# Optimization experiments

Hardware: AMD Instinct MI355X
Metric: run time of the kernel (lower is better)

The kernel has to match this reference:

```python
import jax, jax.numpy as jnp
import numpy as np
from jax.ops import segment_sum, segment_max

N, E, F, H, G, P, C = 50000, 600000, 128, 128, 64, 32, 10
HEADS = 3
BN_EPS = 1e-5
COS_EPS = 1e-8


def setup_inputs() -> dict:
    key = jax.random.key(0)
    ks = jax.random.split(key, 32)
    rn = lambda k, shape, s: jax.random.normal(k, shape, jnp.float32) * s
    inp = {
        "x": jax.random.normal(ks[0], (N, F), jnp.float32),
        "edge_index": jax.random.randint(ks[1], (2, E), 0, N, jnp.int32),
        "batch": jnp.sort(jax.random.randint(ks[2], (N,), 0, G, jnp.int32)),
        # GCNConv
        "W1": rn(ks[3], (F, H), F ** -0.5), "b1": jnp.zeros((H,), jnp.float32),
        # SAGEConv (lin_l on aggregated neighbors, lin_r on root)
        "Wl": rn(ks[4], (H, H), H ** -0.5), "Wr": rn(ks[5], (H, H), H ** -0.5),
        "bs": jnp.zeros((H,), jnp.float32),
        # GATConv, heads=3, concat=False
        "Wg": rn(ks[6], (H, HEADS * H), H ** -0.5),
        "a_src": rn(ks[7], (HEADS, H), H ** -0.5),
        "a_dst": rn(ks[8], (HEADS, H), H ** -0.5),
        "bg": jnp.zeros((H,), jnp.float32),
        # prototype head / classifier / decoder
        "protos": jax.random.normal(ks[9], (P, H), jnp.float32),
        "Wc": rn(ks[10], (H, C), H ** -0.5), "bc": jnp.zeros((C,), jnp.float32),
        "Wd1": rn(ks[11], (H, 2 * H), H ** -0.5), "bd1": jnp.zeros((2 * H,), jnp.float32),
        "Wd2": rn(ks[12], (2 * H, F), (2 * H) ** -0.5), "bd2": jnp.zeros((F,), jnp.float32),
    }
    # BatchNorm (eval mode): gamma, beta, running mean/var for bn1..bn3
    for i in range(3):
        k0, k1, k2 = jax.random.split(ks[13 + i], 3)
        inp[f"g{i+1}"] = 1.0 + rn(k0, (H,), 0.05)
        inp[f"be{i+1}"] = rn(k1, (H,), 0.05)
        inp[f"m{i+1}"] = rn(k2, (H,), 0.1)
        inp[f"v{i+1}"] = jnp.ones((H,), jnp.float32)
    return inp


def _bn(x, g, b, m, v):
    return (x - m) * jax.lax.rsqrt(v + BN_EPS) * g + b


def _forward(x, edge_index, batch,
             W1, b1, g1, be1, m1, v1,
             Wl, Wr, bs, g2, be2, m2, v2,
             Wg, a_src, a_dst, bg, g3, be3, m3, v3,
             protos, Wc, bc, Wd1, bd1, Wd2, bd2):
    src, dst = edge_index[0], edge_index[1]
    ones_e = jnp.ones((src.shape[0],), x.dtype)

    # --- GCNConv: symmetric norm with self-loops ---
    h = x @ W1                                        # [N, H]
    deg = segment_sum(ones_e, dst, num_segments=N) + 1.0
    dinv = jax.lax.rsqrt(deg)
    coef = dinv[src] * dinv[dst]                      # [E]
    h1 = segment_sum(h[src] * coef[:, None], dst, num_segments=N)
    h1 = h1 + h * (dinv * dinv)[:, None] + b1         # self-loop term + bias
    h1 = jax.nn.elu(_bn(h1, g1, be1, m1, v1))         # dropout = identity (eval)

    # --- SAGEConv: mean aggregation (no self-loops) ---
    cnt = segment_sum(ones_e, dst, num_segments=N)
    mean_nb = segment_sum(h1[src], dst, num_segments=N) / jnp.maximum(cnt, 1.0)[:, None]
    h2 = mean_nb @ Wl + h1 @ Wr + bs
    h2 = jax.nn.elu(_bn(h2, g2, be2, m2, v2))

    # --- GATConv: heads=3, concat=False (mean), with self-loops ---
    hg = (h2 @ Wg).reshape(N, HEADS, H)               # [N, 3, H]
    al_src = jnp.einsum('nhf,hf->nh', hg, a_src)      # [N, 3]
    al_dst = jnp.einsum('nhf,hf->nh', hg, a_dst)
    loop = jnp.arange(N, dtype=src.dtype)
    s2 = jnp.concatenate([src, loop])
    d2 = jnp.concatenate([dst, loop])
    e = jax.nn.leaky_relu(al_src[s2] + al_dst[d2], 0.2)   # [E+N, 3]
    emax = segment_max(e, d2, num_segments=N)             # every node has a self-loop
    ex = jnp.exp(e - emax[d2])
    den = segment_sum(ex, d2, num_segments=N)
    alpha = ex / den[d2]                                  # [E+N, 3]
    h3 = segment_sum(hg[s2] * alpha[:, :, None], d2, num_segments=N)
    h3 = h3.mean(axis=1) + bg                             # concat=False -> head mean
    h3 = jax.nn.elu(_bn(h3, g3, be3, m3, v3))

    # --- global mean pool over graphs ---
    gcnt = segment_sum(jnp.ones((N,), x.dtype), batch, num_segments=G)
    pooled = segment_sum(h3, batch, num_segments=G) / jnp.maximum(gcnt, 1.0)[:, None]

    # --- prototype head: cosine sim -> softmax -> mix ---
    xn = pooled / jnp.maximum(jnp.linalg.norm(pooled, axis=-1, keepdims=True), COS_EPS)
    pn = protos / jnp.maximum(jnp.linalg.norm(protos, axis=-1, keepdims=True), COS_EPS)
    sims = xn @ pn.T                                      # [G, P]
    assignments = jax.nn.softmax(sims, axis=-1)
    proto_emb = assignments @ protos                      # [G, H]
    logits = proto_emb @ Wc + bc                          # [G, C]
    reconstructed = jax.nn.relu(pooled @ Wd1 + bd1) @ Wd2 + bd2   # [G, F]
    return logits, proto_emb, assignments, reconstructed


def reference(x, edge_index, batch,
              W1, b1, g1, be1, m1, v1,
              Wl, Wr, bs, g2, be2, m2, v2,
              Wg, a_src, a_dst, bg, g3, be3, m3, v3,
              protos, Wc, bc, Wd1, bd1, Wd2, bd2):
    return _forward(x, edge_index, batch,
                    W1, b1, g1, be1, m1, v1,
                    Wl, Wr, bs, g2, be2, m2, v2,
                    Wg, a_src, a_dst, bg, g3, be3, m3, v3,
                    protos, Wc, bc, Wd1, bd1, Wd2, bd2)
```

## Files before the change

kernel.cpp:

```cpp
#include <hip/hip_runtime.h>
#include <hip/hip_bf16.h>
#include <stdint.h>
#include <stddef.h>

#define N_ 50000
#define E_ 600000
#define F_ 128
#define H_ 128
#define G_ 64
#define P_ 32
#define C_ 10
#define NB_ 49

typedef __hip_bfloat16 bf16;
typedef __attribute__((ext_vector_type(8))) short short8;
typedef __attribute__((ext_vector_type(4))) float float4v;

__device__ __forceinline__ float us2f(unsigned short u){ return __uint_as_float(((unsigned int)u)<<16); }
__device__ __forceinline__ unsigned short f2us(float x){ bf16 h = __float2bfloat16(x); return *(unsigned short*)&h; }
__device__ __forceinline__ float blo(unsigned int u){ return __uint_as_float(u<<16); }
__device__ __forceinline__ float bhi(unsigned int u){ return __uint_as_float(u & 0xFFFF0000u); }
__device__ __forceinline__ unsigned int packbf(float lo, float hi){ return ((unsigned int)f2us(hi)<<16) | f2us(lo); }
__device__ __forceinline__ float eluf(float x){ return x>0.f ? x : __expf(x)-1.f; }
__device__ __forceinline__ float bnf(float x,float m,float v,float g,float b){ return (x-m)*rsqrtf(v+1e-5f)*g+b; }
__device__ __forceinline__ float lrelu(float x){ return x>0.f ? x : 0.2f*x; }
__device__ __forceinline__ float expc(float x){ return __expf(fminf(x, 50.f)); }
__device__ __forceinline__ void atomAddF(float* a, float v){ unsafeAtomicAdd(a, v); }

__global__ __launch_bounds__(256) void k_wprep(const float* __restrict__ W1, const float* __restrict__ Wl,
    const float* __restrict__ Wr, const float* __restrict__ Wg, unsigned short* __restrict__ WT){
  int idx = blockIdx.x*256 + threadIdx.x;
  if(idx >= 6*16384) return;
  int m    = idx >> 14;
  int tile = (idx >> 11) & 7;
  int kc   = (idx >> 9) & 3;
  int lane = (idx >> 3) & 63;
  int j    = idx & 7;
  int k = kc*32 + (lane>>4)*8 + j;
  int n = tile*16 + (lane&15);
  float v;
  if(m==0)      v = W1[k*128+n];
  else if(m==1) v = Wl[k*128+n];
  else if(m==2) v = Wr[k*128+n];
  else          v = Wg[k*384 + (m-3)*128 + n];
  WT[idx] = f2us(v);
}

__global__ __launch_bounds__(384) void k_vprep(const float* __restrict__ Wg, const float* __restrict__ a_src,
    const float* __restrict__ a_dst, float* __restrict__ vs3, float* __restrict__ vd3){
  int t = threadIdx.x;
  if(t >= 384) return;
  int h = t >> 7, f = t & 127;
  const float4* wr = (const float4*)(Wg + (size_t)f*384 + h*128);
  const float4* as = (const float4*)(a_src + h*128);
  const float4* ad = (const float4*)(a_dst + h*128);
  float s = 0.f, d = 0.f;
  #pragma unroll 8
  for(int j=0;j<32;j++){
    float4 wv = wr[j], av = as[j], dv = ad[j];
    s += wv.x*av.x + wv.y*av.y + wv.z*av.z + wv.w*av.w;
    d += wv.x*dv.x + wv.y*dv.y + wv.z*dv.z + wv.w*dv.w;
  }
  vs3[t] = s; vd3[t] = d;
}

__device__ __forceinline__ void load_Afrag_bf16(const bf16* A, int row, int lane, short8 af[4]){
  const unsigned short* ap = (const unsigned short*)A + (size_t)row*128 + (lane>>4)*8;
  #pragma unroll
  for(int kc=0;kc<4;kc++) af[kc] = *(const short8*)(ap + kc*32);
}
__device__ __forceinline__ void mfma_pass_g(const unsigned short* __restrict__ WB, const short8 af[4],
                                            int lane, float4v acc[8]){
  #pragma unroll
  for(int tile=0;tile<8;tile++){
    #pragma unroll
    for(int kc=0;kc<4;kc++){
      short8 bfv = *(const short8*)(WB + (((tile*4+kc)*64 + lane)<<3));
      acc[tile] = __builtin_amdgcn_mfma_f32_16x16x32_bf16(af[kc], bfv, acc[tile], 0, 0, 0);
    }
  }
}

__global__ __launch_bounds__(256) void k_mm_x(const float* __restrict__ X, const unsigned short* __restrict__ WTg,
                                              bf16* __restrict__ HB){
  const int tid = threadIdx.x, lane = tid&63, w = tid>>6;
  const int row0 = blockIdx.x*64;
  int arow = row0 + w*16 + (lane&15);
  int ar = arow < N_ ? arow : N_-1;
  const float* ap = X + (size_t)ar*128 + (lane>>4)*8;
  short8 af[4];
  #pragma unroll
  for(int kc=0;kc<4;kc++){
    float4 a = *(const float4*)(ap + kc*32);
    float4 b = *(const float4*)(ap + kc*32 + 4);
    short8 v;
    v[0]=(short)f2us(a.x); v[1]=(short)f2us(a.y); v[2]=(short)f2us(a.z); v[3]=(short)f2us(a.w);
    v[4]=(short)f2us(b.x); v[5]=(short)f2us(b.y); v[6]=(short)f2us(b.z); v[7]=(short)f2us(b.w);
    af[kc]=v;
  }
  float4v acc[8];
  #pragma unroll
  for(int t=0;t<8;t++){ acc[t][0]=0.f; acc[t][1]=0.f; acc[t][2]=0.f; acc[t][3]=0.f; }
  mfma_pass_g(WTg, af, lane, acc);
  const int colb = lane&15, q = lane>>4;
  unsigned short* ob = (unsigned short*)HB;
  #pragma unroll
  for(int r=0;r<4;r++){
    int ro = row0 + w*16 + q*4 + r;
    if(ro < N_){
      #pragma unroll
      for(int tile=0;tile<8;tile++)
        ob[(size_t)ro*128 + tile*16 + colb] = f2us(acc[tile][r]);
    }
  }
}

__global__ __launch_bounds__(256) void k_sage_mm_att(const bf16* __restrict__ MaB, const bf16* __restrict__ H1B,
    const unsigned short* __restrict__ WlF, const unsigned short* __restrict__ WrF,
    const float* __restrict__ bs, const float* __restrict__ g2, const float* __restrict__ be2,
    const float* __restrict__ m2, const float* __restrict__ v2,
    const float* __restrict__ vs3, const float* __restrict__ vd3,
    bf16* __restrict__ H2B, float* __restrict__ als3, float* __restrict__ ald3){
  const int tid = threadIdx.x, lane = tid&63, w = tid>>6;
  const int row0 = blockIdx.x*64;
  int arow = row0 + w*16 + (lane&15);
  int ar = arow < N_ ? arow : N_-1;
  float4v acc[8];
  #pragma unroll
  for(int t=0;t<8;t++){ acc[t][0]=0.f; acc[t][1]=0.f; acc[t][2]=0.f; acc[t][3]=0.f; }
  short8 af[4];
  load_Afrag_bf16(MaB, ar, lane, af);
  mfma_pass_g(WlF, af, lane, acc);
  load_Afrag_bf16(H1B, ar, lane, af);
  mfma_pass_g(WrF, af, lane, acc);

  const int colb = lane&15, q = lane>>4;
  float vsv[24], vdv[24];
  #pragma unroll
  for(int h=0;h<3;h++){
    #pragma unroll
    for(int tile=0;tile<8;tile++){
      vsv[h*8+tile] = vs3[h*128 + tile*16 + colb];
      vdv[h*8+tile] = vd3[h*128 + tile*16 + colb];
    }
  }
  unsigned short* ob = (unsigned short*)H2B;
  #pragma unroll
  for(int tile=0;tile<8;tile++){
    int col = tile*16 + colb;
    float bsv=bs[col], gv=g2[col], bev=be2[col], mv=m2[col], vv=v2[col];
    #pragma unroll
    for(int r=0;r<4;r++){
      int ro = row0 + w*16 + q*4 + r;
      float x = eluf(bnf(acc[tile][r] + bsv, mv, vv, gv, bev));
      acc[tile][r] = x;
      if(ro < N_) ob[(size_t)ro*128 + col] = f2us(x);
    }
  }
  #pragma unroll
  for(int r=0;r<4;r++){
    int ro = row0 + w*16 + q*4 + r;
    #pragma unroll
    for(int h=0;h<3;h++){
      float ps=0.f, pd=0.f;
      #pragma unroll
      for(int tile=0;tile<8;tile++){ ps += acc[tile][r]*vsv[h*8+tile]; pd += acc[tile][r]*vdv[h*8+tile]; }
      #pragma unroll
      for(int o=8;o>0;o>>=1){ ps += __shfl_down(ps,o,16); pd += __shfl_down(pd,o,16); }
      if(colb==0 && ro<N_){ als3[ro*3+h] = ps; ald3[ro*3+h] = pd; }
    }
  }
}

__global__ __launch_bounds__(256) void k_gat_mm3(const bf16* __restrict__ U, const unsigned short* __restrict__ WgF,
    const float* __restrict__ bg, const float* __restrict__ g3, const float* __restrict__ be3,
    const float* __restrict__ m3, const float* __restrict__ v3, bf16* __restrict__ H3B){
  const int tid = threadIdx.x, lane = tid&63, w = tid>>6;
  const int row0 = blockIdx.x*64;
  int arow = row0 + w*16 + (lane&15);
  int ar = arow < N_ ? arow : N_-1;
  float4v acc[8];
  #pragma unroll
  for(int t=0;t<8;t++){ acc[t][0]=0.f; acc[t][1]=0.f; acc[t][2]=0.f; acc[t][3]=0.f; }
  short8 af[4];
  for(int hh=0; hh<3; hh++){
    const unsigned short* ap = (const unsigned short*)U + (size_t)ar*384 + hh*128 + (lane>>4)*8;
    #pragma unroll
    for(int kc=0;kc<4;kc++) af[kc] = *(const short8*)(ap + kc*32);
    mfma_pass_g(WgF + hh*16384, af, lane, acc);
  }
  const int colb = lane&15, q = lane>>4;
  unsigned short* ob = (unsigned short*)H3B;
  #pragma unroll
  for(int tile=0;tile<8;tile++){
    int col = tile*16 + colb;
    float bgv=bg[col], gv=g3[col], bev=be3[col], mv=m3[col], vv=v3[col];
    #pragma unroll
    for(int r=0;r<4;r++){
      int ro = row0 + w*16 + q*4 + r;
      if(ro < N_){
        float x = acc[tile][r] + bgv;
        ob[(size_t)ro*128 + col] = f2us(eluf(bnf(x, mv, vv, gv, bev)));
      }
    }
  }
}

__global__ __launch_bounds__(256) void k_count(const int* __restrict__ dst, int* __restrict__ cnt){
  int e = blockIdx.x*256 + threadIdx.x;
  if(e < E_) atomicAdd(&cnt[dst[e]], 1);
}

__global__ __launch_bounds__(1024) void k_scan1(const int* __restrict__ cnt, int* __restrict__ row_ptr,
                                                float* __restrict__ dinv, int* __restrict__ bsum){
  __shared__ int wsum[16];
  const int t = threadIdx.x, lane = t & 63, wid = t >> 6;
  int i = blockIdx.x*1024 + t;
  int v = (i<N_) ? cnt[i] : 0;
  int x = v;
  #pragma unroll
  for(int o=1;o<64;o<<=1){
    int y = __shfl_up(x, o, 64);
    if(lane >= o) x += y;
  }
  if(lane==63) wsum[wid] = x;
  __syncthreads();
  if(wid==0){
    int s = (lane<16) ? wsum[lane] : 0;
    #pragma unroll
    for(int o=1;o<16;o<<=1){
      int y = __shfl_up(s, o, 64);
      if(lane >= o) s += y;
    }
    if(lane<16) wsum[lane] = s;
  }
  __syncthreads();
  int waveoff = (wid>0) ? wsum[wid-1] : 0;
  int incl = waveoff + x;
  if(i<N_){
    row_ptr[i] = incl - v;
    dinv[i] = rsqrtf((float)v + 1.f);
  }
  if(t==1023) bsum[blockIdx.x] = incl;
}

__global__ __launch_bounds__(64) void k_scan2(const int* __restrict__ bsum, int* __restrict__ boff,
                                              int* __restrict__ row_ptr){
  int lane = threadIdx.x;
  int v = (lane < NB_) ? bsum[lane] : 0;
  int x = v;
  #pragma unroll
  for(int o=1;o<64;o<<=1){
    int y = __shfl_up(x, o, 64);
    if(lane >= o) x += y;
  }
  if(lane < NB_) boff[lane] = x - v;
  if(lane == 63) row_ptr[N_] = x;
}

__global__ __launch_bounds__(256) void k_scan3(int* __restrict__ row_ptr, const int* __restrict__ boff,
                                               int* __restrict__ tmp){
  int i = blockIdx.x*256 + threadIdx.x;
  if(i < N_){
    int r = row_ptr[i] + boff[i>>10];
    row_ptr[i] = r;
    tmp[i] = r;
  }
}

__global__ __launch_bounds__(256) void k_scatter(const int* __restrict__ src, const int* __restrict__ dst,
                                                 int* __restrict__ tmp, int* __restrict__ esrc,
                                                 int* __restrict__ edst){
  int e = blockIdx.x*256 + threadIdx.x;
  if(e < E_){
    int d = dst[e];
    int pos = atomicAdd(&tmp[d], 1);
    esrc[pos] = src[e];
    edst[pos] = d;
  }
}

__global__ __launch_bounds__(256) void k_wexp(const int* __restrict__ esrc, const int* __restrict__ edst,
    const float* __restrict__ als3, const float* __restrict__ ald3, float* __restrict__ we4){
  int e = blockIdx.x*256 + threadIdx.x;
  if(e >= E_) return;
  int s = esrc[e], d = edst[e];
  float4 w;
  w.x = expc(lrelu(als3[s*3+0] + ald3[d*3+0]));
  w.y = expc(lrelu(als3[s*3+1] + ald3[d*3+1]));
  w.z = expc(lrelu(als3[s*3+2] + ald3[d*3+2]));
  w.w = 0.f;
  *(float4*)(we4 + (size_t)e*4) = w;
}

__global__ __launch_bounds__(256) void k_gcn_gather(const int* __restrict__ row_ptr, const int* __restrict__ esrc,
    const float* __restrict__ dinv, const bf16* __restrict__ HB,
    const float* __restrict__ b1, const float* __restrict__ g1, const float* __restrict__ be1,
    const float* __restrict__ m1, const float* __restrict__ v1, bf16* __restrict__ H1B){
  int n = blockIdx.x*4 + (threadIdx.x>>6);
  int lane = threadIdx.x & 63;
  if(n >= N_) return;
  int beg = row_ptr[n], end = row_ptr[n+1];
  float dn = dinv[n];
  float a0 = 0.f, a1 = 0.f;
  const unsigned short* hb = (const unsigned short*)HB;
  int e = beg;
  for(; e+3 < end; e += 4){
    int s0 = esrc[e], s1 = esrc[e+1], s2 = esrc[e+2], s3 = esrc[e+3];
    unsigned int hv0 = *(const unsigned int*)(hb + (size_t)s0*H_ + lane*2);
    unsigned int hv1 = *(const unsigned int*)(hb + (size_t)s1*H_ + lane*2);
    unsigned int hv2 = *(const unsigned int*)(hb + (size_t)s2*H_ + lane*2);
    unsigned int hv3 = *(const unsigned int*)(hb + (size_t)s3*H_ + lane*2);
    float c0 = dinv[s0]*dn, c1 = dinv[s1]*dn, c2 = dinv[s2]*dn, c3 = dinv[s3]*dn;
    a0 += c0*blo(hv0) + c1*blo(hv1) + c2*blo(hv2) + c3*blo(hv3);
    a1 += c0*bhi(hv0) + c1*bhi(hv1) + c2*bhi(hv2) + c3*bhi(hv3);
  }
  for(; e < end; e++){
    int s = esrc[e];
    float c = dinv[s]*dn;
    unsigned int hv = *(const unsigned int*)(hb + (size_t)s*H_ + lane*2);
    a0 += c*blo(hv);
    a1 += c*bhi(hv);
  }
  unsigned int hv = *(const unsigned int*)(hb + (size_t)n*H_ + lane*2);
  int f0 = lane*2, f1 = f0+1;
  float x0 = a0 + blo(hv)*dn*dn + b1[f0];
  float x1 = a1 + bhi(hv)*dn*dn + b1[f1];
  x0 = eluf(bnf(x0, m1[f0], v1[f0], g1[f0], be1[f0]));
  x1 = eluf(bnf(x1, m1[f1], v1[f1], g1[f1], be1[f1]));
  unsigned int o = ((unsigned int)f2us(x1)<<16) | f2us(x0);
  *(unsigned int*)((unsigned short*)H1B + (size_t)n*H_ + lane*2) = o;
}

__global__ __launch_bounds__(256) void k_sage_gather(const int* __restrict__ row_ptr, const int* __restrict__ esrc,
    const bf16* __restrict__ H1B, bf16* __restrict__ MeanB){
  int n = blockIdx.x*4 + (threadIdx.x>>6);
  int lane = threadIdx.x & 63;
  if(n >= N_) return;
  int beg = row_ptr[n], end = row_ptr[n+1];
  float a0 = 0.f, a1 = 0.f;
  const unsigned short* hb = (const unsigned short*)H1B;
  int e = beg;
  for(; e+3 < end; e += 4){
    int s0 = esrc[e], s1 = esrc[e+1], s2 = esrc[e+2], s3 = esrc[e+3];
    unsigned int hv0 = *(const unsigned int*)(hb + (size_t)s0*H_ + lane*2);
    unsigned int hv1 = *(const unsigned int*)(hb + (size_t)s1*H_ + lane*2);
    unsigned int hv2 = *(const unsigned int*)(hb + (size_t)s2*H_ + lane*2);
    unsigned int hv3 = *(const unsigned int*)(hb + (size_t)s3*H_ + lane*2);
    a0 += blo(hv0) + blo(hv1) + blo(hv2) + blo(hv3);
    a1 += bhi(hv0) + bhi(hv1) + bhi(hv2) + bhi(hv3);
  }
  for(; e < end; e++){
    unsigned int hv = *(const unsigned int*)(hb + (size_t)esrc[e]*H_ + lane*2);
    a0 += blo(hv);
    a1 += bhi(hv);
  }
  float inv = 1.f / fmaxf((float)(end-beg), 1.f);
  unsigned int o = ((unsigned int)f2us(a1*inv)<<16) | f2us(a0*inv);
  *(unsigned int*)((unsigned short*)MeanB + (size_t)n*H_ + lane*2) = o;
}

__global__ __launch_bounds__(256) void k_gat_agg(const int* __restrict__ row_ptr, const int* __restrict__ esrc,
    const float* __restrict__ als3, const float* __restrict__ ald3, const float* __restrict__ we4,
    const bf16* __restrict__ H2B, bf16* __restrict__ U){
  int n = blockIdx.x*4 + (threadIdx.x>>6);
  int lane = threadIdx.x & 63;
  if(n >= N_) return;
  int beg = row_ptr[n], end = row_ptr[n+1];
  float es0 = expc(lrelu(als3[n*3+0] + ald3[n*3+0]));
  float es1 = expc(lrelu(als3[n*3+1] + ald3[n*3+1]));
  float es2 = expc(lrelu(als3[n*3+2] + ald3[n*3+2]));
  const unsigned short* hb = (const unsigned short*)H2B;
  unsigned int xs = *(const unsigned int*)(hb + (size_t)n*H_ + lane*2);
  float x0 = blo(xs), x1 = bhi(xs);
  float den0 = es0, den1 = es1, den2 = es2;
  float a00 = es0*x0, a01 = es0*x1;
  float a10 = es1*x0, a11 = es1*x1;
  float a20 = es2*x0, a21 = es2*x1;
  int e = beg;
  for(; e+3 < end; e += 4){
    int s0 = esrc[e], s1 = esrc[e+1], s2 = esrc[e+2], s3 = esrc[e+3];
    float4 w0 = *(const float4*)(we4 + (size_t)(e  )*4);
    float4 w1 = *(const float4*)(we4 + (size_t)(e+1)*4);
    float4 w2 = *(const float4*)(we4 + (size_t)(e+2)*4);
    float4 w3 = *(const float4*)(we4 + (size_t)(e+3)*4);
    unsigned int p0 = *(const unsigned int*)(hb + (size_t)s0*H_ + lane*2);
    unsigned int p1 = *(const unsigned int*)(hb + (size_t)s1*H_ + lane*2);
    unsigned int p2 = *(const unsigned int*)(hb + (size_t)s2*H_ + lane*2);
    unsigned int p3 = *(const unsigned int*)(hb + (size_t)s3*H_ + lane*2);
    den0 += w0.x + w1.x + w2.x + w3.x;
    den1 += w0.y + w1.y + w2.y + w3.y;
    den2 += w0.z + w1.z + w2.z + w3.z;
    float q00=blo(p0), q01=bhi(p0), q10=blo(p1), q11=bhi(p1);
    float q20=blo(p2), q21=bhi(p2), q30=blo(p3), q31=bhi(p3);
    a00 += w0.x*q00 + w1.x*q10 + w2.x*q20 + w3.x*q30;
    a01 += w0.x*q01 + w1.x*q11 + w2.x*q21 + w3.x*q31;
    a10 += w0.y*q00 + w1.y*q10 + w2.y*q20 + w3.y*q30;
    a11 += w0.y*q01 + w1.y*q11 + w2.y*q21 + w3.y*q31;
    a20 += w0.z*q00 + w1.z*q10 + w2.z*q20 + w3.z*q30;
    a21 += w0.z*q01 + w1.z*q11 + w2.z*q21 + w3.z*q31;
  }
  for(; e < end; e++){
    int s = esrc[e];
    float4 w = *(const float4*)(we4 + (size_t)e*4);
    unsigned int p = *(const unsigned int*)(hb + (size_t)s*H_ + lane*2);
    float q0 = blo(p), q1 = bhi(p);
    den0 += w.x; den1 += w.y; den2 += w.z;
    a00 += w.x*q0; a01 += w.x*q1;
    a10 += w.y*q0; a11 += w.y*q1;
    a20 += w.z*q0; a21 += w.z*q1;
  }
  float i0 = 1.f/(3.f*den0), i1 = 1.f/(3.f*den1), i2 = 1.f/(3.f*den2);
  unsigned short* ub = (unsigned short*)U;
  size_t ubase = (size_t)n*384 + lane*2;
  *(unsigned int*)(ub + ubase)       = packbf(a00*i0, a01*i0);
  *(unsigned int*)(ub + ubase + 128) = packbf(a10*i1, a11*i1);
  *(unsigned int*)(ub + ubase + 256) = packbf(a20*i2, a21*i2);
}

#define NPW_ 16
__global__ __launch_bounds__(256) void k_h3pool(const bf16* __restrict__ H3B,
    const int* __restrict__ batch, float* __restrict__ pooled, float* __restrict__ gcnt){
  int wave = blockIdx.x*4 + (threadIdx.x>>6);
  int lane = threadIdx.x & 63;
  int n0 = wave*NPW_;
  if(n0 >= N_) return;
  int n1 = n0 + NPW_; if(n1 > N_) n1 = N_;
  int f0 = lane*2, f1 = f0+1;
  float r0=0.f, r1=0.f;
  int cur = batch[n0];
  int seg = 0;
  for(int n=n0; n<n1; n++){
    int b = batch[n];
    if(b != cur){
      atomAddF(&pooled[cur*H_ + f0], r0);
      atomAddF(&pooled[cur*H_ + f1], r1);
      if(lane==0) atomAddF(&gcnt[cur], (float)seg);
      r0 = 0.f; r1 = 0.f; seg = 0; cur = b;
    }
    unsigned int hv = *(const unsigned int*)((const unsigned short*)H3B + (size_t)n*H_ + lane*2);
    r0 += blo(hv);
    r1 += bhi(hv);
    seg++;
  }
  atomAddF(&pooled[cur*H_ + f0], r0);
  atomAddF(&pooled[cur*H_ + f1], r1);
  if(lane==0) atomAddF(&gcnt[cur], (float)seg);
}

__global__ __launch_bounds__(128) void k_head(const float* __restrict__ pooledacc, const float* __restrict__ gcnt,
    const float* __restrict__ protos, const float* __restrict__ Wc, const float* __restrict__ bc,
    const float* __restrict__ Wd1, const float* __restrict__ bd1, const float* __restrict__ Wd2, const float* __restrict__ bd2,
    float* __restrict__ out){
  const int g = blockIdx.x, t = threadIdx.x;
  __shared__ float p[128], xn[128], red[128], sims[32], es[32], asg[32], pe[128], t1[256];
  __shared__ float nrm;
  float cg_ = fmaxf(gcnt[g], 1.f);
  p[t] = pooledacc[g*128 + t] / cg_;
  __syncthreads();
  red[t] = p[t]*p[t];
  __syncthreads();
  for(int s=64;s>0;s>>=1){ if(t<s) red[t]+=red[t+s]; __syncthreads(); }
  if(t==0) nrm = fmaxf(sqrtf(red[0]), 1e-8f);
  __syncthreads();
  xn[t] = p[t]/nrm;
  __syncthreads();
  if(t<32){
    float s=0.f, pn=0.f;
    for(int f=0;f<128;f++){ float pv=protos[t*128+f]; s += xn[f]*pv; pn += pv*pv; }
    sims[t] = s / fmaxf(sqrtf(pn), 1e-8f);
  }
  __syncthreads();
  if(t<32){
    float mx=-1e30f;
    for(int j=0;j<32;j++) mx = fmaxf(mx, sims[j]);
    es[t] = __expf(sims[t]-mx);
  }
  __syncthreads();
  if(t<32){
    float sm=0.f;
    for(int j=0;j<32;j++) sm += es[j];
    float a = es[t]/fmaxf(sm,1e-20f);
    asg[t] = a;
    out[8832 + g*32 + t] = a;
  }
  __syncthreads();
  {
    float s=0.f;
    for(int pp=0;pp<32;pp++) s += asg[pp]*protos[pp*128+t];
    pe[t] = s;
    out[640 + g*128 + t] = s;
  }
  __syncthreads();
  if(t<10){
    float s = bc[t];
    for(int f=0;f<128;f++) s += pe[f]*Wc[f*10+t];
    out[g*10 + t] = s;
  }
  for(int j=t;j<256;j+=128){
    float s = bd1[j];
    for(int f=0;f<128;f++) s += p[f]*Wd1[f*256+j];
    t1[j] = fmaxf(s, 0.f);
  }
  __syncthreads();
  {
    float s = bd2[t];
    for(int j=0;j<256;j++) s += t1[j]*Wd2[j*128+t];
    out[10880 + g*128 + t] = s;
  }
}

__global__ void k_sentinel(float* out, float code){
  out[0] = code;
}

extern "C" void kernel_launch(void* const* d_in, const int* in_sizes, int n_in,
                              void* d_out, int out_size, void* d_ws, size_t ws_size,
                              hipStream_t stream){
  const float* X    = (const float*)d_in[0];
  const int*  EI    = (const int*)d_in[1];
  const int*  batch = (const int*)d_in[2];
  const int* src = EI;
  const int* dst = EI + E_;

  int iW1,ib1,iWl,iWr,ibs,iWg,ias,iad,ibg,ipr,iWc,ibc,iWd1,ibd1,iWd2,ibd2;
  int ig1,ibe1,im1,iv1,ig2,ibe2,im2,iv2,ig3,ibe3,im3,iv3;
  if(n_in >= 31 && in_sizes[5] == 128){
    iW1=3; ib1=4; ig1=5; ibe1=6; im1=7; iv1=8;
    iWl=9; iWr=10; ibs=11; ig2=12; ibe2=13; im2=14; iv2=15;
    iWg=16; ias=17; iad=18; ibg=19; ig3=20; ibe3=21; im3=22; iv3=23;
    ipr=24; iWc=25; ibc=26; iWd1=27; ibd1=28; iWd2=29; ibd2=30;
  }else{
    iW1=3; ib1=4; iWl=5; iWr=6; ibs=7; iWg=8; ias=9; iad=10; ibg=11;
    ipr=12; iWc=13; ibc=14; iWd1=15; ibd1=16; iWd2=17; ibd2=18;
    ig1=19; ibe1=20; im1=21; iv1=22; ig2=23; ibe2=24; im2=25; iv2=26;
    ig3=27; ibe3=28; im3=29; iv3=30;
  }
  const float* W1 = (const float*)d_in[iW1];   const float* b1 = (const float*)d_in[ib1];
  const float* Wl = (const float*)d_in[iWl];   const float* Wr = (const float*)d_in[iWr];
  const float* bs = (const float*)d_in[ibs];   const float* Wg = (const float*)d_in[iWg];
  const float* a_src = (const float*)d_in[ias]; const float* a_dst = (const float*)d_in[iad];
  const float* bg = (const float*)d_in[ibg];   const float* protos = (const float*)d_in[ipr];
  const float* Wc = (const float*)d_in[iWc];   const float* bc = (const float*)d_in[ibc];
  const float* Wd1 = (const float*)d_in[iWd1]; const float* bd1 = (const float*)d_in[ibd1];
  const float* Wd2 = (const float*)d_in[iWd2]; const float* bd2 = (const float*)d_in[ibd2];
  const float* g1 = (const float*)d_in[ig1];   const float* be1 = (const float*)d_in[ibe1];
  const float* m1 = (const float*)d_in[im1];   const float* v1 = (const float*)d_in[iv1];
  const float* g2 = (const float*)d_in[ig2];   const float* be2 = (const float*)d_in[ibe2];
  const float* m2 = (const float*)d_in[im2];   const float* v2 = (const float*)d_in[iv2];
  const float* g3 = (const float*)d_in[ig3];   const float* be3 = (const float*)d_in[ibe3];
  const float* m3 = (const float*)d_in[im3];   const float* v3 = (const float*)d_in[iv3];

  const size_t NF = (size_t)N_*H_;
  const size_t intN = (size_t)3*N_ + 4 + (size_t)2*E_ + 128;
  const size_t fltN = (size_t)7*N_ + (size_t)4*E_ + G_*H_ + G_ + 768;
  const size_t NEED = NF*2*3 + (size_t)N_*384*2 + intN*4 + fltN*4 + (size_t)6*16384*2;
  if(ws_size < NEED){
    k_sentinel<<<1,1,0,stream>>>((float*)d_out, 1000.f + (float)(ws_size>>20));
    return;
  }
  bf16* RA = (bf16*)d_ws;
  bf16* RB = RA + NF;
  bf16* RC = RB + NF;
  bf16* U  = RC + NF;
  int*  cnt     = (int*)(U + (size_t)N_*384);
  int*  row_ptr = cnt + N_;
  int*  tmp     = row_ptr + (N_+4);
  int*  esrc    = tmp + N_;
  int*  edst    = esrc + E_;
  int*  bsum    = edst + E_;
  int*  boff    = bsum + 64;
  float* dinv   = (float*)(boff + 64);
  float* als3   = dinv + N_;
  float* ald3   = als3 + (size_t)N_*3;
  float* we4    = ald3 + (size_t)N_*3;
  float* pooled = we4 + (size_t)E_*4;
  float* gcnt   = pooled + (size_t)G_*H_;
  float* vs3    = gcnt + G_;
  float* vd3    = vs3 + 384;
  unsigned short* WTg = (unsigned short*)(vd3 + 384);

  k_wprep<<<(6*16384+255)/256, 256, 0, stream>>>(W1, Wl, Wr, Wg, WTg);
  k_vprep<<<1, 384, 0, stream>>>(Wg, a_src, a_dst, vs3, vd3);
  hipMemsetAsync(cnt, 0, N_*sizeof(int), stream);
  k_count<<<(E_+255)/256, 256, 0, stream>>>(dst, cnt);
  k_scan1<<<NB_, 1024, 0, stream>>>(cnt, row_ptr, dinv, bsum);
  k_scan2<<<1, 64, 0, stream>>>(bsum, boff, row_ptr);
  k_scan3<<<(N_+255)/256, 256, 0, stream>>>(row_ptr, boff, tmp);
  k_scatter<<<(E_+255)/256, 256, 0, stream>>>(src, dst, tmp, esrc, edst);

  const int GB = (N_+3)/4;
  const int MB = (N_+63)/64;
  k_mm_x<<<MB, 256, 0, stream>>>(X, WTg, RA);
  k_gcn_gather<<<GB, 256, 0, stream>>>(row_ptr, esrc, dinv, RA, b1, g1, be1, m1, v1, RB);
  k_sage_gather<<<GB, 256, 0, stream>>>(row_ptr, esrc, RB, RC);
  k_sage_mm_att<<<MB, 256, 0, stream>>>(RC, RB, WTg + 16384, WTg + 2*16384, bs, g2, be2, m2, v2,
                                        vs3, vd3, RA, als3, ald3);
  k_wexp<<<(E_+255)/256, 256, 0, stream>>>(esrc, edst, als3, ald3, we4);
  k_gat_agg<<<GB, 256, 0, stream>>>(row_ptr, esrc, als3, ald3, we4, RA, U);
  k_gat_mm3<<<MB, 256, 0, stream>>>(U, WTg + 3*16384, bg, g3, be3, m3, v3, RC);
  hipMemsetAsync(pooled, 0, (size_t)(G_*H_+G_)*sizeof(float), stream);
  {
    int waves = (N_ + NPW_ - 1)/NPW_;
    int blocks = (waves + 3)/4;
    k_h3pool<<<blocks, 256, 0, stream>>>(RC, batch, pooled, gcnt);
  }
  k_head<<<G_, 128, 0, stream>>>(pooled, gcnt, protos, Wc, bc, Wd1, bd1, Wd2, bd2, (float*)d_out);
}
```

Measured before the change: 427.5 us.

## Fuse GAT edge-weight computation into aggregation with wave-cooperative index loads

Removes the separate edge-weight kernel and its per-edge float4 weight array, computing attention weights inside the GAT aggregation. Each lane loads one neighbor index and its source logits, computes the exp weights, then broadcasts them with shuffles. Attention logits are padded to 4 floats per node so they can be read as one float4, and the edst array is no longer written in the scatter. This cuts one launch and the write-then-read traffic of the weight array, at the cost of extra shuffles and redundant exp work per edge chunk.

```diff
diff --git a/kernel.cpp b/kernel.cpp
--- a/kernel.cpp
+++ b/kernel.cpp
@@ -120,7 +120,7 @@
     const float* __restrict__ bs, const float* __restrict__ g2, const float* __restrict__ be2,
     const float* __restrict__ m2, const float* __restrict__ v2,
     const float* __restrict__ vs3, const float* __restrict__ vd3,
-    bf16* __restrict__ H2B, float* __restrict__ als3, float* __restrict__ ald3){
+    bf16* __restrict__ H2B, float* __restrict__ als4, float* __restrict__ ald4){
   const int tid = threadIdx.x, lane = tid&63, w = tid>>6;
   const int row0 = blockIdx.x*64;
   int arow = row0 + w*16 + (lane&15);
@@ -167,7 +167,7 @@
       for(int tile=0;tile<8;tile++){ ps += acc[tile][r]*vsv[h*8+tile]; pd += acc[tile][r]*vdv[h*8+tile]; }
       #pragma unroll
       for(int o=8;o>0;o>>=1){ ps += __shfl_down(ps,o,16); pd += __shfl_down(pd,o,16); }
-      if(colb==0 && ro<N_){ als3[ro*3+h] = ps; ald3[ro*3+h] = pd; }
+      if(colb==0 && ro<N_){ als4[ro*4+h] = ps; ald4[ro*4+h] = pd; }
     }
   }
 }
@@ -269,28 +269,13 @@
 }
 
 __global__ __launch_bounds__(256) void k_scatter(const int* __restrict__ src, const int* __restrict__ dst,
-                                                 int* __restrict__ tmp, int* __restrict__ esrc,
-                                                 int* __restrict__ edst){
+                                                 int* __restrict__ tmp, int* __restrict__ esrc){
   int e = blockIdx.x*256 + threadIdx.x;
   if(e < E_){
     int d = dst[e];
     int pos = atomicAdd(&tmp[d], 1);
     esrc[pos] = src[e];
-    edst[pos] = d;
-  }
-}
-
-__global__ __launch_bounds__(256) void k_wexp(const int* __restrict__ esrc, const int* __restrict__ edst,
-    const float* __restrict__ als3, const float* __restrict__ ald3, float* __restrict__ we4){
-  int e = blockIdx.x*256 + threadIdx.x;
-  if(e >= E_) return;
-  int s = esrc[e], d = edst[e];
-  float4 w;
-  w.x = expc(lrelu(als3[s*3+0] + ald3[d*3+0]));
-  w.y = expc(lrelu(als3[s*3+1] + ald3[d*3+1]));
-  w.z = expc(lrelu(als3[s*3+2] + ald3[d*3+2]));
-  w.w = 0.f;
-  *(float4*)(we4 + (size_t)e*4) = w;
+  }
 }
 
 __global__ __launch_bounds__(256) void k_gcn_gather(const int* __restrict__ row_ptr, const int* __restrict__ esrc,
@@ -361,15 +346,17 @@
 }
 
 __global__ __launch_bounds__(256) void k_gat_agg(const int* __restrict__ row_ptr, const int* __restrict__ esrc,
-    const float* __restrict__ als3, const float* __restrict__ ald3, const float* __restrict__ we4,
+    const float* __restrict__ als4, const float* __restrict__ ald4,
     const bf16* __restrict__ H2B, bf16* __restrict__ U){
   int n = blockIdx.x*4 + (threadIdx.x>>6);
   int lane = threadIdx.x & 63;
   if(n >= N_) return;
   int beg = row_ptr[n], end = row_ptr[n+1];
-  float es0 = expc(lrelu(als3[n*3+0] + ald3[n*3+0]));
-  float es1 = expc(lrelu(als3[n*3+1] + ald3[n*3+1]));
-  float es2 = expc(lrelu(als3[n*3+2] + ald3[n*3+2]));
+  float4 asn = *(const float4*)(als4 + (size_t)n*4);
+  float4 adn = *(const float4*)(ald4 + (size_t)n*4);
+  float es0 = expc(lrelu(asn.x + adn.x));
+  float es1 = expc(lrelu(asn.y + adn.y));
+  float es2 = expc(lrelu(asn.z + adn.z));
   const unsigned short* hb = (const unsigned short*)H2B;
   unsigned int xs = *(const unsigned int*)(hb + (size_t)n*H_ + lane*2);
   float x0 = blo(xs), x1 = bhi(xs);
@@ -377,38 +364,46 @@
   float a00 = es0*x0, a01 = es0*x1;
   float a10 = es1*x0, a11 = es1*x1;
   float a20 = es2*x0, a21 = es2*x1;
-  int e = beg;
-  for(; e+3 < end; e += 4){
-    int s0 = esrc[e], s1 = esrc[e+1], s2 = esrc[e+2], s3 = esrc[e+3];
-    float4 w0 = *(const float4*)(we4 + (size_t)(e  )*4);
-    float4 w1 = *(const float4*)(we4 + (size_t)(e+1)*4);
-    float4 w2 = *(const float4*)(we4 + (size_t)(e+2)*4);
-    float4 w3 = *(const float4*)(we4 + (size_t)(e+3)*4);
-    unsigned int p0 = *(const unsigned int*)(hb + (size_t)s0*H_ + lane*2);
-    unsigned int p1 = *(const unsigned int*)(hb + (size_t)s1*H_ + lane*2);
-    unsigned int p2 = *(const unsigned int*)(hb + (size_t)s2*H_ + lane*2);
-    unsigned int p3 = *(const unsigned int*)(hb + (size_t)s3*H_ + lane*2);
-    den0 += w0.x + w1.x + w2.x + w3.x;
-    den1 += w0.y + w1.y + w2.y + w3.y;
-    den2 += w0.z + w1.z + w2.z + w3.z;
-    float q00=blo(p0), q01=bhi(p0), q10=blo(p1), q11=bhi(p1);
-    float q20=blo(p2), q21=bhi(p2), q30=blo(p3), q31=bhi(p3);
-    a00 += w0.x*q00 + w1.x*q10 + w2.x*q20 + w3.x*q30;
-    a01 += w0.x*q01 + w1.x*q11 + w2.x*q21 + w3.x*q31;
-    a10 += w0.y*q00 + w1.y*q10 + w2.y*q20 + w3.y*q30;
-    a11 += w0.y*q01 + w1.y*q11 + w2.y*q21 + w3.y*q31;
-    a20 += w0.z*q00 + w1.z*q10 + w2.z*q20 + w3.z*q30;
-    a21 += w0.z*q01 + w1.z*q11 + w2.z*q21 + w3.z*q31;
-  }
-  for(; e < end; e++){
-    int s = esrc[e];
-    float4 w = *(const float4*)(we4 + (size_t)e*4);
-    unsigned int p = *(const unsigned int*)(hb + (size_t)s*H_ + lane*2);
-    float q0 = blo(p), q1 = bhi(p);
-    den0 += w.x; den1 += w.y; den2 += w.z;
-    a00 += w.x*q0; a01 += w.x*q1;
-    a10 += w.y*q0; a11 += w.y*q1;
-    a20 += w.z*q0; a21 += w.z*q1;
+  for(int c = beg; c < end; c += 64){
+    int take = end - c; if(take > 64) take = 64;
+    int idx = esrc[c + (lane < take ? lane : take-1)];
+    float4 asl = *(const float4*)(als4 + (size_t)idx*4);
+    float w0l = expc(lrelu(asl.x + adn.x));
+    float w1l = expc(lrelu(asl.y + adn.y));
+    float w2l = expc(lrelu(asl.z + adn.z));
+    int j = 0;
+    for(; j+3 < take; j += 4){
+      int s0=__shfl(idx,j),  s1=__shfl(idx,j+1),  s2=__shfl(idx,j+2),  s3=__shfl(idx,j+3);
+      float u00=__shfl(w0l,j),   u01=__shfl(w1l,j),   u02=__shfl(w2l,j);
+      float u10=__shfl(w0l,j+1), u11=__shfl(w1l,j+1), u12=__shfl(w2l,j+1);
+      float u20=__shfl(w0l,j+2), u21=__shfl(w1l,j+2), u22=__shfl(w2l,j+2);
+      float u30=__shfl(w0l,j+3), u31=__shfl(w1l,j+3), u32=__shfl(w2l,j+3);
+      unsigned int p0 = *(const unsigned int*)(hb + (size_t)s0*H_ + lane*2);
+      unsigned int p1 = *(const unsigned int*)(hb + (size_t)s1*H_ + lane*2);
+      unsigned int p2 = *(const unsigned int*)(hb + (size_t)s2*H_ + lane*2);
+      unsigned int p3 = *(const unsigned int*)(hb + (size_t)s3*H_ + lane*2);
+      den0 += u00 + u10 + u20 + u30;
+      den1 += u01 + u11 + u21 + u31;
+      den2 += u02 + u12 + u22 + u32;
+      float q00=blo(p0), q01=bhi(p0), q10=blo(p1), q11=bhi(p1);
+      float q20=blo(p2), q21=bhi(p2), q30=blo(p3), q31=bhi(p3);
+      a00 += u00*q00 + u10*q10 + u20*q20 + u30*q30;
+      a01 += u00*q01 + u10*q11 + u20*q21 + u30*q31;
+      a10 += u01*q00 + u11*q10 + u21*q20 + u31*q30;
+      a11 += u01*q01 + u11*q11 + u21*q21 + u31*q31;
+      a20 += u02*q00 + u12*q10 + u22*q20 + u32*q30;
+      a21 += u02*q01 + u12*q11 + u22*q21 + u32*q31;
+    }
+    for(; j < take; j++){
+      int s = __shfl(idx,j);
+      float u0=__shfl(w0l,j), u1=__shfl(w1l,j), u2=__shfl(w2l,j);
+      unsigned int p = *(const unsigned int*)(hb + (size_t)s*H_ + lane*2);
+      float q0 = blo(p), q1 = bhi(p);
+      den0 += u0; den1 += u1; den2 += u2;
+      a00 += u0*q0; a01 += u0*q1;
+      a10 += u1*q0; a11 += u1*q1;
+      a20 += u2*q0; a21 += u2*q1;
+    }
   }
   float i0 = 1.f/(3.f*den0), i1 = 1.f/(3.f*den1), i2 = 1.f/(3.f*den2);
   unsigned short* ub = (unsigned short*)U;
@@ -552,8 +547,8 @@
   const float* m3 = (const float*)d_in[im3];   const float* v3 = (const float*)d_in[iv3];
 
   const size_t NF = (size_t)N_*H_;
-  const size_t intN = (size_t)3*N_ + 4 + (size_t)2*E_ + 128;
-  const size_t fltN = (size_t)7*N_ + (size_t)4*E_ + G_*H_ + G_ + 768;
+  const size_t intN = (size_t)3*N_ + 4 + (size_t)E_ + 128;
+  const size_t fltN = (size_t)9*N_ + G_*H_ + G_ + 768;
   const size_t NEED = NF*2*3 + (size_t)N_*384*2 + intN*4 + fltN*4 + (size_t)6*16384*2;
   if(ws_size < NEED){
     k_sentinel<<<1,1,0,stream>>>((float*)d_out, 1000.f + (float)(ws_size>>20));
@@ -567,14 +562,12 @@
   int*  row_ptr = cnt + N_;
   int*  tmp     = row_ptr + (N_+4);
   int*  esrc    = tmp + N_;
-  int*  edst    = esrc + E_;
-  int*  bsum    = edst + E_;
+  int*  bsum    = esrc + E_;
   int*  boff    = bsum + 64;
   float* dinv   = (float*)(boff + 64);
-  float* als3   = dinv + N_;
-  float* ald3   = als3 + (size_t)N_*3;
-  float* we4    = ald3 + (size_t)N_*3;
-  float* pooled = we4 + (size_t)E_*4;
+  float* als4   = dinv + N_;
+  float* ald4   = als4 + (size_t)N_*4;
+  float* pooled = ald4 + (size_t)N_*4;
   float* gcnt   = pooled + (size_t)G_*H_;
   float* vs3    = gcnt + G_;
   float* vd3    = vs3 + 384;
@@ -583,11 +576,12 @@
   k_wprep<<<(6*16384+255)/256, 256, 0, stream>>>(W1, Wl, Wr, Wg, WTg);
   k_vprep<<<1, 384, 0, stream>>>(Wg, a_src, a_dst, vs3, vd3);
   hipMemsetAsync(cnt, 0, N_*sizeof(int), stream);
+  hipMemsetAsync(pooled, 0, (size_t)(G_*H_+G_)*sizeof(float), stream);
   k_count<<<(E_+255)/256, 256, 0, stream>>>(dst, cnt);
   k_scan1<<<NB_, 1024, 0, stream>>>(cnt, row_ptr, dinv, bsum);
   k_scan2<<<1, 64, 0, stream>>>(bsum, boff, row_ptr);
   k_scan3<<<(N_+255)/256, 256, 0, stream>>>(row_ptr, boff, tmp);
-  k_scatter<<<(E_+255)/256, 256, 0, stream>>>(src, dst, tmp, esrc, edst);
+  k_scatter<<<(E_+255)/256, 256, 0, stream>>>(src, dst, tmp, esrc);
 
   const int GB = (N_+3)/4;
   const int MB = (N_+63)/64;
@@ -595,11 +589,9 @@
   k_gcn_gather<<<GB, 256, 0, stream>>>(row_ptr, esrc, dinv, RA, b1, g1, be1, m1, v1, RB);
   k_sage_gather<<<GB, 256, 0, stream>>>(row_ptr, esrc, RB, RC);
   k_sage_mm_att<<<MB, 256, 0, stream>>>(RC, RB, WTg + 16384, WTg + 2*16384, bs, g2, be2, m2, v2,
-                                        vs3, vd3, RA, als3, ald3);
-  k_wexp<<<(E_+255)/256, 256, 0, stream>>>(esrc, edst, als3, ald3, we4);
-  k_gat_agg<<<GB, 256, 0, stream>>>(row_ptr, esrc, als3, ald3, we4, RA, U);
+                                        vs3, vd3, RA, als4, ald4);
+  k_gat_agg<<<GB, 256, 0, stream>>>(row_ptr, esrc, als4, ald4, RA, U);
   k_gat_mm3<<<MB, 256, 0, stream>>>(U, WTg + 3*16384, bg, g3, be3, m3, v3, RC);
-  hipMemsetAsync(pooled, 0, (size_t)(G_*H_+G_)*sizeof(float), stream);
   {
     int waves = (N_ + NPW_ - 1)/NPW_;
     int blocks = (waves + 3)/4;
```

Result: faster. 414.5 us (-3.1%).
